# Kernel optimization log

Hardware: AMD Instinct MI355X
Metric: run time of the kernel (lower is better)

## Reference

```python
import jax, jax.numpy as jnp
import numpy as np

NUM_ITERS = 3


def squash(s, axis=-1):
    # v = (|s|^2 / (1+|s|^2)) * s / |s|
    sq = jnp.sum(s * s, axis=axis, keepdims=True)
    return sq / (1.0 + sq) * s / jnp.sqrt(sq)


def setup_inputs() -> dict:
    key = jax.random.key(0)
    k1, k2 = jax.random.split(key)
    B, C, R, I, O = 256, 10, 1152, 8, 16
    x = jax.random.normal(k1, (B, R, I), dtype=jnp.float32)
    route_weights = jax.random.normal(k2, (C, R, I, O), dtype=jnp.float32)
    return {"x": x, "route_weights": route_weights}


def reference(x, route_weights):
    # x: [B, R, I]; route_weights: [C, R, I, O]
    # u: predictions from each route node for each output capsule: [B, C, R, 1, O]
    u = jnp.einsum("bri,crio->bcro", x, route_weights)[:, :, :, None, :]
    b = jnp.zeros_like(u)
    v = None
    for i in range(NUM_ITERS):
        c = jax.nn.softmax(b, axis=2)          # softmax over route nodes (dim=2)
        s = jnp.sum(c * u, axis=2, keepdims=True)  # [B, C, 1, 1, O]
        v = squash(s, axis=-1)
        if i != NUM_ITERS - 1:
            b = b + jnp.sum(u * v, axis=-1, keepdims=True)  # agreement, broadcast over O
    return v  # [B, C, 1, 1, O]
```

## Files before the change

kernel.cpp:

```cpp
#include <hip/hip_runtime.h>


#define B_ 256
#define C_ 10
#define R_ 1152
#define I_ 8
#define O_ 16
#define T_ 512
#define BPB 4
#define RPP 128
#define KPT 9
#define NW 8
#define NITER 3

__device__ __forceinline__ uint32_t bf16_rn(float f) {
    uint32_t u = __builtin_bit_cast(uint32_t, f);
    return (u + 0x7FFFu + ((u >> 16) & 1u)) >> 16;
}
__device__ __forceinline__ uint32_t pack2(float lo, float hi) {
    return bf16_rn(lo) | (bf16_rn(hi) << 16);
}
__device__ __forceinline__ float unlo(uint32_t p) {
    return __builtin_bit_cast(float, p << 16);
}
__device__ __forceinline__ float unhi(uint32_t p) {
    return __builtin_bit_cast(float, p & 0xFFFF0000u);
}

__global__ __launch_bounds__(T_, 2) void capsule_routing_kernel(
    const float* __restrict__ x,
    const float* __restrict__ w,
    float* __restrict__ out)
{
    const int wg   = blockIdx.x;
    const int c    = wg >> 6;
    const int b0   = (wg & 63) * BPB;
    const int tid  = threadIdx.x;
    const int lane = tid & 63;
    const int wid  = tid >> 6;
    const int oq   = tid & 3;
    const int rl   = tid >> 2;

    __shared__ float sred[BPB][NW][4][4];
    __shared__ float zred[BPB][NW];
    __shared__ float vsum[BPB][O_];

    uint32_t up[BPB][KPT][2];

    if (tid < BPB * O_) vsum[tid >> 4][tid & 15] = 0.f;

    #pragma unroll
    for (int k = 0; k < KPT; ++k) {
        const int r = k * RPP + rl;
        const float4* wb4 = (const float4*)(w + ((size_t)c * R_ + r) * (I_ * O_));
        float4 W0 = wb4[0 * 4 + oq], W1 = wb4[1 * 4 + oq];
        float4 W2 = wb4[2 * 4 + oq], W3 = wb4[3 * 4 + oq];
        float4 W4 = wb4[4 * 4 + oq], W5 = wb4[5 * 4 + oq];
        float4 W6 = wb4[6 * 4 + oq], W7 = wb4[7 * 4 + oq];
        #pragma unroll
        for (int bb = 0; bb < BPB; ++bb) {
            const float4* xp = (const float4*)(x + ((size_t)(b0 + bb) * R_ + r) * I_);
            const float4 xa = xp[0];
            const float4 xb = xp[1];
            float a0, a1, a2, a3;
            a0 = xa.x * W0.x; a1 = xa.x * W0.y; a2 = xa.x * W0.z; a3 = xa.x * W0.w;
            a0 += xa.y * W1.x; a1 += xa.y * W1.y; a2 += xa.y * W1.z; a3 += xa.y * W1.w;
            a0 += xa.z * W2.x; a1 += xa.z * W2.y; a2 += xa.z * W2.z; a3 += xa.z * W2.w;
            a0 += xa.w * W3.x; a1 += xa.w * W3.y; a2 += xa.w * W3.z; a3 += xa.w * W3.w;
            a0 += xb.x * W4.x; a1 += xb.x * W4.y; a2 += xb.x * W4.z; a3 += xb.x * W4.w;
            a0 += xb.y * W5.x; a1 += xb.y * W5.y; a2 += xb.y * W5.z; a3 += xb.y * W5.w;
            a0 += xb.z * W6.x; a1 += xb.z * W6.y; a2 += xb.z * W6.z; a3 += xb.z * W6.w;
            a0 += xb.w * W7.x; a1 += xb.w * W7.y; a2 += xb.w * W7.z; a3 += xb.w * W7.w;
            up[bb][k][0] = pack2(a0, a1);
            up[bb][k][1] = pack2(a2, a3);
        }
    }
    __syncthreads();

    #pragma unroll
    for (int it = 0; it < NITER; ++it) {
        float zz[BPB], ss[BPB][4];
        #pragma unroll
        for (int bb = 0; bb < BPB; ++bb) {
            float4 vs = make_float4(0.f, 0.f, 0.f, 0.f);
            if (it > 0) vs = *(const float4*)&vsum[bb][oq * 4];
            float z = 0.f, s0 = 0.f, s1 = 0.f, s2 = 0.f, s3 = 0.f;
            #pragma unroll
            for (int k = 0; k < KPT; ++k) {
                const float u0 = unlo(up[bb][k][0]);
                const float u1 = unhi(up[bb][k][0]);
                const float u2 = unlo(up[bb][k][1]);
                const float u3 = unhi(up[bb][k][1]);
                float e;
                if (it == 0) {
                    e = 1.f;
                } else {
                    float d = u0 * vs.x + u1 * vs.y + u2 * vs.z + u3 * vs.w;
                    d += __shfl_xor(d, 1);
                    d += __shfl_xor(d, 2);
                    e = __expf(d);
                }
                z += e;
                s0 += e * u0; s1 += e * u1; s2 += e * u2; s3 += e * u3;
            }
            zz[bb] = z;
            ss[bb][0] = s0; ss[bb][1] = s1; ss[bb][2] = s2; ss[bb][3] = s3;
        }
        #pragma unroll
        for (int off = 4; off <= 32; off <<= 1) {
            #pragma unroll
            for (int bb = 0; bb < BPB; ++bb) {
                zz[bb] += __shfl_xor(zz[bb], off);
                ss[bb][0] += __shfl_xor(ss[bb][0], off);
                ss[bb][1] += __shfl_xor(ss[bb][1], off);
                ss[bb][2] += __shfl_xor(ss[bb][2], off);
                ss[bb][3] += __shfl_xor(ss[bb][3], off);
            }
        }
        if (lane < 4) {
            #pragma unroll
            for (int bb = 0; bb < BPB; ++bb) {
                sred[bb][wid][lane][0] = ss[bb][0];
                sred[bb][wid][lane][1] = ss[bb][1];
                sred[bb][wid][lane][2] = ss[bb][2];
                sred[bb][wid][lane][3] = ss[bb][3];
                if (lane == 0) zred[bb][wid] = zz[bb];
            }
        }
        __syncthreads();

        if (wid == 0) {
            const int bb = lane >> 4;
            const int o  = lane & 15;
            float S = 0.f, Z = 0.f;
            #pragma unroll
            for (int wv = 0; wv < NW; ++wv) {
                S += sred[bb][wv][o >> 2][o & 3];
                Z += zred[bb][wv];
            }
            const float inv = 1.f / Z;
            const float svn = S * inv;
            float p = svn * svn;
            p += __shfl_xor(p, 1);
            p += __shfl_xor(p, 2);
            p += __shfl_xor(p, 4);
            p += __shfl_xor(p, 8);
            const float scale = sqrtf(p) / (1.f + p);
            const float vf = svn * scale;
            vsum[bb][o] += vf;
            if (it == NITER - 1)
                out[((size_t)(b0 + bb) * C_ + c) * O_ + o] = vf;
        }
        if (it != NITER - 1) __syncthreads();
    }
}

extern "C" void kernel_launch(void* const* d_in, const int* in_sizes, int n_in,
                              void* d_out, int out_size, void* d_ws, size_t ws_size,
                              hipStream_t stream) {
    const float* x = (const float*)d_in[0];
    const float* w = (const float*)d_in[1];
    float* out = (float*)d_out;
    capsule_routing_kernel<<<dim3(C_ * (B_ / BPB)), dim3(T_), 0, stream>>>(x, w, out);
}
```

Baseline: 70.57 us.

## Split capsule routing into prediction kernel and per-(batch,class) routing kernel

Computes the bf16-packed prediction vectors u in a separate kernel that loads each weight slice once and loops over 32 batches, storing u to workspace. A second kernel then runs one block per (batch, class) for the routing iterations, raising parallelism and reducing per-thread register state. This trades redundant weight reads for a large workspace write and read-back of u. The old fused kernel remains as a fallback when the workspace is too small.

```diff
diff --git a/kernel.cpp b/kernel.cpp
--- a/kernel.cpp
+++ b/kernel.cpp
@@ -1,4 +1,5 @@
 #include <hip/hip_runtime.h>
+#include <stdint.h>
 
 
 #define B_ 256
@@ -7,8 +8,6 @@
 #define I_ 8
 #define O_ 16
 #define T_ 512
-#define BPB 4
-#define RPP 128
 #define KPT 9
 #define NW 8
 #define NITER 3
@@ -27,7 +26,136 @@
     return __builtin_bit_cast(float, p & 0xFFFF0000u);
 }
 
-__global__ __launch_bounds__(T_, 2) void capsule_routing_kernel(
+__global__ __launch_bounds__(T_, 2) void caps_u_kernel(
+    const float* __restrict__ x,
+    const float* __restrict__ w,
+    uint2* __restrict__ u)
+{
+    const int bx  = blockIdx.x;
+    const int c   = bx / 72;
+    const int kc  = (bx % 72) >> 3;
+    const int bt  = bx & 7;
+    const int tid = threadIdx.x;
+    const int oq  = tid & 3;
+    const int rl  = tid >> 2;
+    const int r   = kc * 128 + rl;
+
+    const float4* wb4 = (const float4*)(w + ((size_t)c * R_ + r) * (I_ * O_));
+    const float4 W0 = wb4[0 * 4 + oq], W1 = wb4[1 * 4 + oq];
+    const float4 W2 = wb4[2 * 4 + oq], W3 = wb4[3 * 4 + oq];
+    const float4 W4 = wb4[4 * 4 + oq], W5 = wb4[5 * 4 + oq];
+    const float4 W6 = wb4[6 * 4 + oq], W7 = wb4[7 * 4 + oq];
+
+    #pragma unroll 4
+    for (int bb = 0; bb < 32; ++bb) {
+        const int b = bt * 32 + bb;
+        const float4* xp = (const float4*)(x + ((size_t)b * R_ + r) * I_);
+        const float4 xa = xp[0];
+        const float4 xb = xp[1];
+        float a0, a1, a2, a3;
+        a0 = xa.x * W0.x; a1 = xa.x * W0.y; a2 = xa.x * W0.z; a3 = xa.x * W0.w;
+        a0 += xa.y * W1.x; a1 += xa.y * W1.y; a2 += xa.y * W1.z; a3 += xa.y * W1.w;
+        a0 += xa.z * W2.x; a1 += xa.z * W2.y; a2 += xa.z * W2.z; a3 += xa.z * W2.w;
+        a0 += xa.w * W3.x; a1 += xa.w * W3.y; a2 += xa.w * W3.z; a3 += xa.w * W3.w;
+        a0 += xb.x * W4.x; a1 += xb.x * W4.y; a2 += xb.x * W4.z; a3 += xb.x * W4.w;
+        a0 += xb.y * W5.x; a1 += xb.y * W5.y; a2 += xb.y * W5.z; a3 += xb.y * W5.w;
+        a0 += xb.z * W6.x; a1 += xb.z * W6.y; a2 += xb.z * W6.z; a3 += xb.z * W6.w;
+        a0 += xb.w * W7.x; a1 += xb.w * W7.y; a2 += xb.w * W7.z; a3 += xb.w * W7.w;
+        u[(((size_t)b * C_ + c) * KPT + kc) * T_ + tid] =
+            make_uint2(pack2(a0, a1), pack2(a2, a3));
+    }
+}
+
+__global__ __launch_bounds__(T_, 2) void caps_route_kernel(
+    const uint2* __restrict__ u,
+    float* __restrict__ out)
+{
+    const int wg   = blockIdx.x;
+    const int tid  = threadIdx.x;
+    const int lane = tid & 63;
+    const int wid  = tid >> 6;
+    const int oq   = tid & 3;
+
+    __shared__ float sred[NW][4][4];
+    __shared__ float zred[NW];
+    __shared__ float vsum[O_];
+
+    uint2 up[KPT];
+    #pragma unroll
+    for (int k = 0; k < KPT; ++k)
+        up[k] = u[((size_t)wg * KPT + k) * T_ + tid];
+
+    if (tid < O_) vsum[tid] = 0.f;
+    __syncthreads();
+
+    #pragma unroll
+    for (int it = 0; it < NITER; ++it) {
+        float4 vs = make_float4(0.f, 0.f, 0.f, 0.f);
+        if (it > 0) vs = *(const float4*)&vsum[oq * 4];
+        float z = 0.f, s0 = 0.f, s1 = 0.f, s2 = 0.f, s3 = 0.f;
+        #pragma unroll
+        for (int k = 0; k < KPT; ++k) {
+            const float u0 = unlo(up[k].x);
+            const float u1 = unhi(up[k].x);
+            const float u2 = unlo(up[k].y);
+            const float u3 = unhi(up[k].y);
+            float e;
+            if (it == 0) {
+                e = 1.f;
+            } else {
+                float d = u0 * vs.x + u1 * vs.y + u2 * vs.z + u3 * vs.w;
+                d += __shfl_xor(d, 1);
+                d += __shfl_xor(d, 2);
+                e = __expf(d);
+            }
+            z += e;
+            s0 += e * u0; s1 += e * u1; s2 += e * u2; s3 += e * u3;
+        }
+        #pragma unroll
+        for (int off = 4; off <= 32; off <<= 1) {
+            z  += __shfl_xor(z, off);
+            s0 += __shfl_xor(s0, off);
+            s1 += __shfl_xor(s1, off);
+            s2 += __shfl_xor(s2, off);
+            s3 += __shfl_xor(s3, off);
+        }
+        if (lane < 4) {
+            sred[wid][lane][0] = s0;
+            sred[wid][lane][1] = s1;
+            sred[wid][lane][2] = s2;
+            sred[wid][lane][3] = s3;
+            if (lane == 0) zred[wid] = z;
+        }
+        __syncthreads();
+
+        if (wid == 0 && lane < O_) {
+            float S = 0.f, Z = 0.f;
+            #pragma unroll
+            for (int wv = 0; wv < NW; ++wv) {
+                S += sred[wv][lane >> 2][lane & 3];
+                Z += zred[wv];
+            }
+            const float inv = 1.f / Z;
+            const float svn = S * inv;
+            float p = svn * svn;
+            p += __shfl_xor(p, 1);
+            p += __shfl_xor(p, 2);
+            p += __shfl_xor(p, 4);
+            p += __shfl_xor(p, 8);
+            const float scale = sqrtf(p) / (1.f + p);
+            const float vf = svn * scale;
+            vsum[lane] += vf;
+            if (it == NITER - 1)
+                out[(size_t)wg * O_ + lane] = vf;
+        }
+        if (it != NITER - 1) __syncthreads();
+    }
+}
+
+#define BPB 4
+#define RPP 128
+
+__global__ __launch_bounds__(T_, 2) void capsule_fused_kernel(
     const float* __restrict__ x,
     const float* __restrict__ w,
     float* __restrict__ out)
@@ -161,5 +289,13 @@
     const float* x = (const float*)d_in[0];
     const float* w = (const float*)d_in[1];
     float* out = (float*)d_out;
-    capsule_routing_kernel<<<dim3(C_ * (B_ / BPB)), dim3(T_), 0, stream>>>(x, w, out);
-}
+
+    const size_t u_bytes = (size_t)B_ * C_ * KPT * T_ * 8;
+    if (ws_size >= u_bytes) {
+        uint2* u = (uint2*)d_ws;
+        caps_u_kernel<<<dim3(C_ * KPT * 8), dim3(T_), 0, stream>>>(x, w, u);
+        caps_route_kernel<<<dim3(B_ * C_), dim3(T_), 0, stream>>>(u, out);
+    } else {
+        capsule_fused_kernel<<<dim3(C_ * (B_ / BPB)), dim3(T_), 0, stream>>>(x, w, out);
+    }
+}
```

Result: faster. 65.45 us (-7.3%).
